# Kernel optimization log

Measured on AMD Instinct MI355X. Metric: run time of the kernel, lower is better.

Reference implementation:

```python
import jax, jax.numpy as jnp
import numpy as np

NUM_EXPERTS = 8
TOP_K = 2
HIDDEN = 2048
INTER = 5632
NUM_TOKENS = 8192


def setup_inputs() -> dict:
    key = jax.random.key(0)
    ks = jax.random.split(key, 5)
    s_h = 1.0 / np.sqrt(HIDDEN)
    s_i = 1.0 / np.sqrt(INTER)
    return {
        "hidden_states": jax.random.normal(ks[0], (NUM_TOKENS, HIDDEN), jnp.float32),
        # router: ReplicatedLinear(hidden, num_experts, bias=False) -> weight [E, H]
        "w_router": jax.random.normal(ks[1], (NUM_EXPERTS, HIDDEN), jnp.float32) * s_h,
        # FusedMoE SiLU-gated MLP per expert: gate/up [E, H, I], down [E, I, H]
        "w_gate": jax.random.normal(ks[2], (NUM_EXPERTS, HIDDEN, INTER), jnp.float32) * s_h,
        "w_up": jax.random.normal(ks[3], (NUM_EXPERTS, HIDDEN, INTER), jnp.float32) * s_h,
        "w_down": jax.random.normal(ks[4], (NUM_EXPERTS, INTER, HIDDEN), jnp.float32) * s_i,
    }


def reference(hidden_states, w_router, w_gate, w_up, w_down):
    x = hidden_states  # [T, H]
    # Router linear (no bias)
    router_logits = x @ w_router.T  # [T, E]
    # FusedMoE topk: softmax over all experts, take top-k, renormalize=False
    probs = jax.nn.softmax(router_logits.astype(jnp.float32), axis=-1)
    topk_w, topk_idx = jax.lax.top_k(probs, TOP_K)  # [T, k]
    topk_w = topk_w.astype(x.dtype)

    out = jnp.zeros_like(x)
    for e in range(NUM_EXPERTS):
        # combine weight for tokens that routed to expert e (0 otherwise)
        w_e = jnp.sum(jnp.where(topk_idx == e, topk_w, 0.0), axis=-1)  # [T]
        h = jax.nn.silu(x @ w_gate[e]) * (x @ w_up[e])  # [T, I]
        out = out + (h @ w_down[e]) * w_e[:, None]
    return out
```

## Files before the change

kernel.cpp:

```cpp
#include <hip/hip_runtime.h>
#include <hip/hip_bf16.h>
#include <cstdint>

#define NTOK 8192
#define NEXP 8
#define HID  2048
#define INTR 5632
#define NT1  44
#define NT2  16

#define TCNT_OFF    4096u
#define SLOT_OFF    65536u
#define T2S_OFF     262144u
#define W2_OFF      393216u
#define LISTS_OFF   524288u
#define WL_OFF      786432u
#define WG_OFF      2097152u
#define WBYTES      184549376u
#define WU_OFF      (WG_OFF + WBYTES)
#define HF_OFF      (WU_OFF + WBYTES)
#define HFBYTES     207618048u
#define XG_OFF      (HF_OFF + HFBYTES)

typedef float f32x4  __attribute__((ext_vector_type(4)));
typedef short s16x8  __attribute__((ext_vector_type(8)));
typedef short s16x4  __attribute__((ext_vector_type(4)));

__device__ __forceinline__ short bfc(float f) {
  __hip_bfloat16 h = __float2bfloat16(f);
  return __builtin_bit_cast(short, h);
}
__device__ __forceinline__ float b2f(short s) {
  unsigned u = ((unsigned)(unsigned short)s) << 16;
  return __builtin_bit_cast(float, u);
}
__device__ __forceinline__ s16x8 pk8(float4 a, float4 b) {
  s16x8 v;
  v[0]=bfc(a.x); v[1]=bfc(a.y); v[2]=bfc(a.z); v[3]=bfc(a.w);
  v[4]=bfc(b.x); v[5]=bfc(b.y); v[6]=bfc(b.z); v[7]=bfc(b.w);
  return v;
}
__device__ __forceinline__ void gload16(const void* g, void* l) {
  __builtin_amdgcn_global_load_lds((const __attribute__((address_space(1))) void*)g,
                                   (__attribute__((address_space(3))) void*)l, 16, 0, 0);
}

#define DSR128(dst, addr, IMM) \
  asm volatile("ds_read_b128 %0, %1 offset:" IMM : "=v"(dst) : "v"(addr))
#define WAITLGKM(N) do { \
  asm volatile("s_waitcnt lgkmcnt(" #N ")" ::: "memory"); \
  __builtin_amdgcn_sched_barrier(0); } while (0)
#define WAITVM(N) do { \
  asm volatile("s_waitcnt vmcnt(" #N ")" ::: "memory"); \
  __builtin_amdgcn_sched_barrier(0); } while (0)

#define LOADA4(D0, D1, D2, D3, PTR) \
  asm volatile("global_load_dwordx4 %0, %4, off\n\t" \
               "global_load_dwordx4 %1, %4, off offset:1024\n\t" \
               "global_load_dwordx4 %2, %4, off offset:2048\n\t" \
               "global_load_dwordx4 %3, %4, off offset:3072" \
               : "=&v"(D0), "=&v"(D1), "=&v"(D2), "=&v"(D3) : "v"(PTR))

#define MFMA_BF16 __builtin_amdgcn_mfma_f32_16x16x32_bf16

__global__ __launch_bounds__(256, 4) void prep_kernel(
    const float* __restrict__ src, short* __restrict__ dst,
    int KT, int NP, int Nsrc) {
  __shared__ float tile[32 * 132];
  const int b = blockIdx.x;
  const int np = b % NP;
  const int kt = (b / NP) % KT;
  const int e  = b / (NP * KT);
  const int tid = threadIdx.x;
  const float* s = src + (size_t)e * KT * 32 * (size_t)Nsrc + (size_t)kt * 32 * Nsrc + np * 128;
#pragma unroll
  for (int i = 0; i < 4; i++) {
    const int idx = tid + i * 256;
    const int row = idx >> 5, c4 = idx & 31;
    float4 v = *(const float4*)(s + (size_t)row * Nsrc + c4 * 4);
    *(float4*)(tile + row * 132 + c4 * 4) = v;
  }
  __syncthreads();
  short* dbase = dst + ((size_t)(e * KT + kt) * (NP * 8) + np * 8) * 512;
#pragma unroll
  for (int i = 0; i < 2; i++) {
    const int c = tid + i * 256;
    const int lane = c & 63;
    const int nf = c >> 6;
    const int n = nf * 16 + (lane & 15);
    const int kb = (lane >> 4) * 8;
    s16x8 o;
#pragma unroll
    for (int j = 0; j < 8; j++) o[j] = bfc(tile[(kb + j) * 132 + n]);
    *(s16x8*)(dbase + (size_t)c * 8) = o;
  }
}

__global__ void router_kernel(const float* __restrict__ x, const float* __restrict__ wr,
                              int* __restrict__ cnt, int* __restrict__ lists,
                              float* __restrict__ wlists) {
  const int wave = threadIdx.x >> 6;
  const int lane = threadIdx.x & 63;
  const int t = blockIdx.x * 4 + wave;
  if (t >= NTOK) return;
  float acc[NEXP];
#pragma unroll
  for (int e = 0; e < NEXP; e++) acc[e] = 0.f;
  const float* xrow = x + (size_t)t * HID;
#pragma unroll
  for (int j = 0; j < HID / 256; j++) {
    const int k = j * 256 + lane * 4;
    float4 xv = *(const float4*)(xrow + k);
#pragma unroll
    for (int e = 0; e < NEXP; e++) {
      float4 wv = *(const float4*)(wr + e * HID + k);
      acc[e] += xv.x * wv.x + xv.y * wv.y + xv.z * wv.z + xv.w * wv.w;
    }
  }
#pragma unroll
  for (int e = 0; e < NEXP; e++) {
    float v = acc[e];
    for (int off = 32; off; off >>= 1) v += __shfl_xor(v, off, 64);
    acc[e] = v;
  }
  if (lane == 0) {
    float m = acc[0];
#pragma unroll
    for (int e = 1; e < NEXP; e++) m = fmaxf(m, acc[e]);
    float p[NEXP], s = 0.f;
#pragma unroll
    for (int e = 0; e < NEXP; e++) { p[e] = __expf(acc[e] - m); s += p[e]; }
    const float inv = 1.f / s;
    int e1 = 0; float b1 = p[0];
#pragma unroll
    for (int e = 1; e < NEXP; e++) if (p[e] > b1) { b1 = p[e]; e1 = e; }
    int e2 = -1; float b2 = -1.f;
#pragma unroll
    for (int e = 0; e < NEXP; e++) if (e != e1 && p[e] > b2) { b2 = p[e]; e2 = e; }
    const int pos1 = atomicAdd(&cnt[e1], 1);
    lists[e1 * NTOK + pos1] = t; wlists[e1 * NTOK + pos1] = b1 * inv;
    const int pos2 = atomicAdd(&cnt[e2], 1);
    lists[e2 * NTOK + pos2] = t; wlists[e2 * NTOK + pos2] = b2 * inv;
  }
}

__global__ void offsets_kernel(const int* __restrict__ cnt, int* __restrict__ poffs) {
  if (threadIdx.x == 0 && blockIdx.x == 0) {
    int o = 0;
#pragma unroll
    for (int e = 0; e < NEXP; e++) { poffs[e] = o; o += ((cnt[e] + 255) >> 8) << 8; }
    poffs[NEXP] = o;
  }
}

__global__ void slotmap_kernel(const int* __restrict__ cnt, const int* __restrict__ poffs,
                               const int* __restrict__ lists, const float* __restrict__ wlists,
                               int* __restrict__ slotlist, int* __restrict__ tcnt,
                               int* __restrict__ tok2slot, float* __restrict__ w2) {
  const int e = blockIdx.x;
  const int c = cnt[e], base = poffs[e];
  for (int pos = threadIdx.x; pos < c; pos += blockDim.x) {
    const int tok = lists[e * NTOK + pos];
    const int slot = base + pos;
    slotlist[slot] = tok;
    const int j = atomicAdd(&tcnt[tok], 1);
    tok2slot[tok * 2 + j] = slot;
    w2[tok * 2 + j] = wlists[e * NTOK + pos];
  }
}

__global__ __launch_bounds__(256, 4) void gather_kernel(
    const float* __restrict__ x, const int* __restrict__ slotlist,
    short* __restrict__ xg) {
  const int c = blockIdx.x * 256 + threadIdx.x;
  const int cl = c & 63;
  const int fragid = c >> 6;
  const int f = fragid & 15;
  const int kt = (fragid >> 4) & 63;
  const int gmt = fragid >> 10;
  const int tok = slotlist[gmt * 256 + f * 16 + (cl & 15)];
  const float* s = x + (size_t)tok * HID + kt * 32 + (cl >> 4) * 8;
  float4 a = *(const float4*)s, b = *(const float4*)(s + 4);
  *(s16x8*)(xg + (size_t)c * 8) = pk8(a, b);
}

__global__ __launch_bounds__(512, 2) void gemm1_kernel(
    const short* __restrict__ xg, const short* __restrict__ wgb,
    const short* __restrict__ wub, const int* __restrict__ cnt,
    const int* __restrict__ poffs, short* __restrict__ hfrag) {
  const int P = blockIdx.x;
  const int xcd = P & 7, slot = P >> 3;
  const int mt = slot & 31, jj = slot >> 5;
  const int g = jj * 8 + xcd;
  const int e = g / NT1, nt = g % NT1;
  if (mt * 256 >= cnt[e]) return;
  const int gmt = (poffs[e] >> 8) + mt;
  const int tid = threadIdx.x;
  const int w = tid >> 6, lane = tid & 63;
  const int wm = w >> 1, wn = w & 1;

  __shared__ __align__(16) short Lds[34816];
  const uint32_t ldsbase = (uint32_t)(uintptr_t)&Lds[0];

  const short* srcA  = xg + (size_t)gmt * 64 * 16 * 512 + (size_t)(wm * 4) * 512 + lane * 8;
  const short* srcBg = wgb + (((size_t)e * 64) * 352 + nt * 8) * 512 + tid * 8;
  const short* srcBu = wub + (((size_t)e * 64) * 352 + nt * 8) * 512 + tid * 8;

  const uint32_t roB = wn * 4096 + lane * 16;
  const uint32_t roU = 8192 + wn * 4096 + lane * 16;

  f32x4 accG[4][4], accU[4][4];
#pragma unroll
  for (int i = 0; i < 4; i++)
#pragma unroll
    for (int j = 0; j < 4; j++) {
      accG[i][j] = f32x4{0.f, 0.f, 0.f, 0.f};
      accU[i][j] = f32x4{0.f, 0.f, 0.f, 0.f};
    }

  s16x8 arA0, arA1, arA2, arA3, arB0, arB1, arB2, arB3;

#define STG1(WB) do {                                                           \
    short* d = (short*)Lds + ((WB) >> 1);                                       \
    gload16(srcBg, d + w * 512);                                                \
    gload16(srcBu, d + 4096 + w * 512);                                         \
    srcBg += 180224; srcBu += 180224; } while (0)

#define MMQ1(NF, BG, BU, A0, A1, A2, A3)                                        \
  { __builtin_amdgcn_s_setprio(1);                                              \
    accG[0][NF] = MFMA_BF16(A0, BG, accG[0][NF], 0, 0, 0);                      \
    accU[0][NF] = MFMA_BF16(A0, BU, accU[0][NF], 0, 0, 0);                      \
    accG[1][NF] = MFMA_BF16(A1, BG, accG[1][NF], 0, 0, 0);                      \
    accU[1][NF] = MFMA_BF16(A1, BU, accU[1][NF], 0, 0, 0);                      \
    accG[2][NF] = MFMA_BF16(A2, BG, accG[2][NF], 0, 0, 0);                      \
    accU[2][NF] = MFMA_BF16(A2, BU, accU[2][NF], 0, 0, 0);                      \
    accG[3][NF] = MFMA_BF16(A3, BG, accG[3][NF], 0, 0, 0);                      \
    accU[3][NF] = MFMA_BF16(A3, BU, accU[3][NF], 0, 0, 0);                      \
    __builtin_amdgcn_s_setprio(0); }

#define G1_BODY(RB, WB, U0, U1, U2, U3, L0, L1, L2, L3, VTOP, VMID, DO_A, DO_STG) \
  {                                                                             \
    WAITVM(VTOP);                                                               \
    __builtin_amdgcn_s_barrier();                                               \
    const uint32_t rb = ldsbase + (RB);                                         \
    s16x8 bg0, bg1, bg2, bg3, bu0, bu1, bu2, bu3;                               \
    DSR128(bg0, rb + roB, "0");    DSR128(bu0, rb + roU, "0");                  \
    DSR128(bg1, rb + roB, "1024"); DSR128(bu1, rb + roU, "1024");               \
    DSR128(bg2, rb + roB, "2048"); DSR128(bu2, rb + roU, "2048");               \
    DSR128(bg3, rb + roB, "3072"); DSR128(bu3, rb + roU, "3072");               \
    if (DO_A) { LOADA4(L0, L1, L2, L3, srcA); srcA += 8192; }                   \
    if (DO_STG) { STG1(WB); }                                                   \
    WAITVM(VMID);                                                               \
    WAITLGKM(6);                                                                \
    MMQ1(0, bg0, bu0, U0, U1, U2, U3)                                           \
    WAITLGKM(4);                                                                \
    MMQ1(1, bg1, bu1, U0, U1, U2, U3)                                           \
    WAITLGKM(2);                                                                \
    MMQ1(2, bg2, bu2, U0, U1, U2, U3)                                           \
    WAITLGKM(0);                                                                \
    MMQ1(3, bg3, bu3, U0, U1, U2, U3)                                           \
  }

  STG1(0);
  LOADA4(arA0, arA1, arA2, arA3, srcA); srcA += 8192;
  STG1(16384);

  for (int it = 0; it < 10; ++it) {
    G1_BODY(0,     32768, arA0,arA1,arA2,arA3, arB0,arB1,arB2,arB3, 6, 8, 1, 1)
    G1_BODY(16384, 0,     arB0,arB1,arB2,arB3, arA0,arA1,arA2,arA3, 6, 8, 1, 1)
    G1_BODY(32768, 16384, arA0,arA1,arA2,arA3, arB0,arB1,arB2,arB3, 6, 8, 1, 1)
    G1_BODY(0,     32768, arB0,arB1,arB2,arB3, arA0,arA1,arA2,arA3, 6, 8, 1, 1)
    G1_BODY(16384, 0,     arA0,arA1,arA2,arA3, arB0,arB1,arB2,arB3, 6, 8, 1, 1)
    G1_BODY(32768, 16384, arB0,arB1,arB2,arB3, arA0,arA1,arA2,arA3, 6, 8, 1, 1)
  }
  G1_BODY(0,     32768, arA0,arA1,arA2,arA3, arB0,arB1,arB2,arB3, 6, 8, 1, 1)
  G1_BODY(16384, 0,     arB0,arB1,arB2,arB3, arA0,arA1,arA2,arA3, 6, 8, 1, 1)
  G1_BODY(32768, 0,     arA0,arA1,arA2,arA3, arB0,arB1,arB2,arB3, 6, 6, 1, 0)
  G1_BODY(0,     0,     arB0,arB1,arB2,arB3, arA0,arA1,arA2,arA3, 4, 0, 0, 0)
#undef G1_BODY
#undef MMQ1
#undef STG1

  short* tr = (short*)Lds;
  __syncthreads();
#pragma unroll
  for (int mf = 0; mf < 4; mf++)
#pragma unroll
    for (int reg = 0; reg < 4; reg++) {
      const int row = wm * 64 + mf * 16 + (lane >> 4) * 4 + reg;
#pragma unroll
      for (int nf = 0; nf < 4; nf++) {
        const int col = wn * 64 + nf * 16 + (lane & 15);
        const float gv = accG[mf][nf][reg];
        const float uv = accU[mf][nf][reg];
        tr[row * 136 + col] = bfc((gv / (1.f + __expf(-gv))) * uv);
      }
    }
  __syncthreads();
  short* hb = hfrag + (((size_t)gmt * 176 + nt * 4) * 16) * 512;
#pragma unroll
  for (int i = 0; i < 8; i++) {
    const int c = tid + i * 512;
    const int cl = c & 63;
    const int f = (c >> 6) & 15;
    const int ktl = c >> 10;
    const int rr = f * 16 + (cl & 15);
    s16x8 v = *(const s16x8*)(tr + rr * 136 + ktl * 32 + (cl >> 4) * 8);
    *(s16x8*)(hb + ((size_t)ktl * 16 + f) * 512 + cl * 8) = v;
  }
}

__global__ __launch_bounds__(512, 4) void gemm2_kernel(
    const short* __restrict__ hfrag, const short* __restrict__ wdb,
    const int* __restrict__ cnt, const int* __restrict__ poffs,
    __hip_bfloat16* __restrict__ pout) {
  const int P = blockIdx.x;
  const int xcd = P & 7, r = P >> 3;
  const int nt = r & 15, emq = r >> 4;
  const int gm = emq * 8 + xcd;
  const int e = gm >> 5, mt = gm & 31;
  if (mt * 256 >= cnt[e]) return;
  const int gmt = (poffs[e] >> 8) + mt;
  const int n0 = nt * 128;
  const int tid = threadIdx.x;
  const int w = tid >> 6, lane = tid & 63;
  const int wm = w >> 1, wn = w & 1;

  __shared__ __align__(16) short Lds[3 * 12288];
  const uint32_t ldsbase = (uint32_t)(uintptr_t)&Lds[0];

  const short* srcA = hfrag + (size_t)gmt * 176 * 16 * 512 + tid * 8;
  const short* srcB = wdb + (((size_t)e * 176) * 128 + nt * 8) * 512 + tid * 8;

  const uint32_t roA = wm * 4096 + lane * 16;
  const uint32_t roB = 16384 + wn * 4096 + lane * 16;

  f32x4 acc[4][4];
#pragma unroll
  for (int i = 0; i < 4; i++)
#pragma unroll
    for (int j = 0; j < 4; j++) acc[i][j] = f32x4{0.f, 0.f, 0.f, 0.f};

#define STG2(WB) do {                                                           \
    short* d = (short*)Lds + ((WB) >> 1);                                       \
    gload16(srcA,        d + w * 512);                                          \
    gload16(srcA + 4096, d + 4096 + w * 512);                                   \
    gload16(srcB,        d + 8192 + w * 512);                                   \
    srcA += 8192; srcB += 65536; } while (0)

#define MMQ2(NF, BF)                                                            \
  { __builtin_amdgcn_s_setprio(1);                                              \
    acc[0][NF] = MFMA_BF16(af0, BF, acc[0][NF], 0, 0, 0);                       \
    acc[1][NF] = MFMA_BF16(af1, BF, acc[1][NF], 0, 0, 0);                       \
    acc[2][NF] = MFMA_BF16(af2, BF, acc[2][NF], 0, 0, 0);                       \
    acc[3][NF] = MFMA_BF16(af3, BF, acc[3][NF], 0, 0, 0);                       \
    __builtin_amdgcn_s_setprio(0); }

#define G2_BODY(RB, WB, VMN, DOSTG)                                             \
  {                                                                             \
    WAITVM(VMN);                                                                \
    __builtin_amdgcn_s_barrier();                                               \
    const uint32_t rb = ldsbase + (RB);                                         \
    s16x8 af0, af1, af2, af3, bf0, bf1, bf2, bf3;                               \
    DSR128(bf0, rb + roB, "0");                                                 \
    DSR128(af0, rb + roA, "0");    DSR128(af1, rb + roA, "1024");               \
    DSR128(af2, rb + roA, "2048"); DSR128(af3, rb + roA, "3072");               \
    DSR128(bf1, rb + roB, "1024");                                              \
    DSR128(bf2, rb + roB, "2048");                                              \
    DSR128(bf3, rb + roB, "3072");                                              \
    if (DOSTG) { STG2(WB); }                                                    \
    WAITLGKM(3);                                                                \
    MMQ2(0, bf0)                                                                \
    WAITLGKM(2);                                                                \
    MMQ2(1, bf1)                                                                \
    WAITLGKM(1);                                                                \
    MMQ2(2, bf2)                                                                \
    WAITLGKM(0);                                                                \
    MMQ2(3, bf3)                                                                \
  }

  STG2(0);
  STG2(24576);
  for (int it = 0; it < 58; ++it) {
    G2_BODY(0,     49152, 3, 1)
    G2_BODY(24576, 0,     3, 1)
    G2_BODY(49152, 24576, 3, 1)
  }
  G2_BODY(0,     0, 3, 0)
  G2_BODY(24576, 0, 0, 0)
#undef G2_BODY
#undef MMQ2
#undef STG2

  const int slotb = poffs[e] + mt * 256;
#pragma unroll
  for (int mf = 0; mf < 4; mf++) {
#pragma unroll
    for (int reg = 0; reg < 4; reg++) {
      const int row = wm * 64 + mf * 16 + (lane >> 4) * 4 + reg;
      __hip_bfloat16* op = pout + (size_t)(slotb + row) * HID + n0 + wn * 64 + (lane & 15);
#pragma unroll
      for (int nf = 0; nf < 4; nf++)
        op[nf * 16] = __float2bfloat16(acc[mf][nf][reg]);
    }
  }
}

__global__ __launch_bounds__(256, 8) void combine_kernel(
    const __hip_bfloat16* __restrict__ pout, const int* __restrict__ tok2slot,
    const float* __restrict__ w2, float* __restrict__ out) {
  const int t = blockIdx.x;
  const int s0 = tok2slot[2 * t], s1 = tok2slot[2 * t + 1];
  const float w0 = w2[2 * t], w1 = w2[2 * t + 1];
  const short* p0 = (const short*)pout + (size_t)s0 * HID;
  const short* p1 = (const short*)pout + (size_t)s1 * HID;
  float* o = out + (size_t)t * HID;
  const int i = threadIdx.x;
  s16x8 a = *(const s16x8*)(p0 + i * 8);
  s16x8 b = *(const s16x8*)(p1 + i * 8);
  float4 r0, r1;
  r0.x = w0 * b2f(a[0]) + w1 * b2f(b[0]);
  r0.y = w0 * b2f(a[1]) + w1 * b2f(b[1]);
  r0.z = w0 * b2f(a[2]) + w1 * b2f(b[2]);
  r0.w = w0 * b2f(a[3]) + w1 * b2f(b[3]);
  r1.x = w0 * b2f(a[4]) + w1 * b2f(b[4]);
  r1.y = w0 * b2f(a[5]) + w1 * b2f(b[5]);
  r1.z = w0 * b2f(a[6]) + w1 * b2f(b[6]);
  r1.w = w0 * b2f(a[7]) + w1 * b2f(b[7]);
  *(float4*)(o + i * 8) = r0;
  *(float4*)(o + i * 8 + 4) = r1;
}

extern "C" void kernel_launch(void* const* d_in, const int* in_sizes, int n_in,
                              void* d_out, int out_size, void* d_ws, size_t ws_size,
                              hipStream_t stream) {
  const float* x  = (const float*)d_in[0];
  const float* wr = (const float*)d_in[1];
  const float* wg = (const float*)d_in[2];
  const float* wu = (const float*)d_in[3];
  const float* wd = (const float*)d_in[4];
  float* out = (float*)d_out;
  char* ws = (char*)d_ws;

  int* cnt      = (int*)ws;
  int* poffs    = (int*)(ws + 64);
  int* tcnt     = (int*)(ws + TCNT_OFF);
  int* slotlist = (int*)(ws + SLOT_OFF);
  int* tok2slot = (int*)(ws + T2S_OFF);
  float* w2     = (float*)(ws + W2_OFF);
  int* lists    = (int*)(ws + LISTS_OFF);
  float* wlists = (float*)(ws + WL_OFF);
  short* wgb    = (short*)(ws + WG_OFF);
  short* wub    = (short*)(ws + WU_OFF);
  short* wdb    = (short*)(ws + WG_OFF);
  short* hfrag  = (short*)(ws + HF_OFF);
  short* xg     = (short*)(ws + XG_OFF);
  __hip_bfloat16* pout = (__hip_bfloat16*)(ws + XG_OFF);

  hipMemsetAsync(ws, 0, 256, stream);
  hipMemsetAsync(ws + TCNT_OFF, 0, 32768, stream);
  hipMemsetAsync(ws + SLOT_OFF, 0, 73728, stream);

  router_kernel<<<NTOK / 4, 256, 0, stream>>>(x, wr, cnt, lists, wlists);
  offsets_kernel<<<1, 64, 0, stream>>>(cnt, poffs);
  slotmap_kernel<<<NEXP, 256, 0, stream>>>(cnt, poffs, lists, wlists, slotlist, tcnt, tok2slot, w2);
  gather_kernel<<<18432, 256, 0, stream>>>(x, slotlist, xg);
  prep_kernel<<<NEXP * 64 * 44, 256, 0, stream>>>(wg, wgb, 64, 44, INTR);
  prep_kernel<<<NEXP * 64 * 44, 256, 0, stream>>>(wu, wub, 64, 44, INTR);
  gemm1_kernel<<<8 * 32 * NT1, 512, 0, stream>>>(xg, wgb, wub, cnt, poffs, hfrag);
  prep_kernel<<<NEXP * 176 * 16, 256, 0, stream>>>(wd, wdb, 176, 16, HID);
  gemm2_kernel<<<8 * 16 * 32, 512, 0, stream>>>(hfrag, wdb, cnt, poffs, pout);
  combine_kernel<<<NTOK, 256, 0, stream>>>(pout, tok2slot, w2, out);
}
```

Measured before the change: 1.677 ms.

## Double wavefronts per block in both MoE GEMMs, halving per-wave N tile

Both grouped GEMM kernels now launch 1024 threads (16 waves) instead of 512. Each wave computes a 64x32 output slice instead of 64x64, which halves accumulator registers and B-fragment LDS reads per wave. gemm2 now loads A directly from global memory into registers, as gemm1 already does, instead of staging it in LDS, which shrinks its LDS buffers. The aim is more resident waves for latency hiding, at the cost of more redundant A loads, more barrier participants, and lower MFMA work per wave relative to LDS traffic.

```diff
diff --git a/kernel.cpp b/kernel.cpp
--- a/kernel.cpp
+++ b/kernel.cpp
@@ -184,7 +184,7 @@
   *(s16x8*)(xg + (size_t)c * 8) = pk8(a, b);
 }
 
-__global__ __launch_bounds__(512, 2) void gemm1_kernel(
+__global__ __launch_bounds__(1024, 4) void gemm1_kernel(
     const short* __restrict__ xg, const short* __restrict__ wgb,
     const short* __restrict__ wub, const int* __restrict__ cnt,
     const int* __restrict__ poffs, short* __restrict__ hfrag) {
@@ -197,23 +197,24 @@
   const int gmt = (poffs[e] >> 8) + mt;
   const int tid = threadIdx.x;
   const int w = tid >> 6, lane = tid & 63;
-  const int wm = w >> 1, wn = w & 1;
+  const int wm = w >> 2, wn = w & 3;
 
   __shared__ __align__(16) short Lds[34816];
   const uint32_t ldsbase = (uint32_t)(uintptr_t)&Lds[0];
 
-  const short* srcA  = xg + (size_t)gmt * 64 * 16 * 512 + (size_t)(wm * 4) * 512 + lane * 8;
-  const short* srcBg = wgb + (((size_t)e * 64) * 352 + nt * 8) * 512 + tid * 8;
-  const short* srcBu = wub + (((size_t)e * 64) * 352 + nt * 8) * 512 + tid * 8;
-
-  const uint32_t roB = wn * 4096 + lane * 16;
-  const uint32_t roU = 8192 + wn * 4096 + lane * 16;
-
-  f32x4 accG[4][4], accU[4][4];
+  const short* srcA = xg + (size_t)gmt * 64 * 16 * 512 + (size_t)(wm * 4) * 512 + lane * 8;
+  const int stid = tid & 511;
+  const short* srcB = ((tid < 512) ? wgb : wub)
+                    + (((size_t)e * 64) * 352 + nt * 8) * 512 + stid * 8;
+
+  const uint32_t roB = wn * 2048 + lane * 16;
+  const uint32_t roU = 8192 + wn * 2048 + lane * 16;
+
+  f32x4 accG[4][2], accU[4][2];
 #pragma unroll
   for (int i = 0; i < 4; i++)
 #pragma unroll
-    for (int j = 0; j < 4; j++) {
+    for (int j = 0; j < 2; j++) {
       accG[i][j] = f32x4{0.f, 0.f, 0.f, 0.f};
       accU[i][j] = f32x4{0.f, 0.f, 0.f, 0.f};
     }
@@ -221,10 +222,8 @@
   s16x8 arA0, arA1, arA2, arA3, arB0, arB1, arB2, arB3;
 
 #define STG1(WB) do {                                                           \
-    short* d = (short*)Lds + ((WB) >> 1);                                       \
-    gload16(srcBg, d + w * 512);                                                \
-    gload16(srcBu, d + 4096 + w * 512);                                         \
-    srcBg += 180224; srcBu += 180224; } while (0)
+    gload16(srcB, (short*)Lds + ((WB) >> 1) + tid * 8);                         \
+    srcB += 180224; } while (0)
 
 #define MMQ1(NF, BG, BU, A0, A1, A2, A3)                                        \
   { __builtin_amdgcn_s_setprio(1);                                              \
@@ -238,27 +237,20 @@
     accU[3][NF] = MFMA_BF16(A3, BU, accU[3][NF], 0, 0, 0);                      \
     __builtin_amdgcn_s_setprio(0); }
 
-#define G1_BODY(RB, WB, U0, U1, U2, U3, L0, L1, L2, L3, VTOP, VMID, DO_A, DO_STG) \
+#define G1_BODY(RB, WB, U0, U1, U2, U3, L0, L1, L2, L3, VTOP, DO_A, DO_STG)     \
   {                                                                             \
     WAITVM(VTOP);                                                               \
     __builtin_amdgcn_s_barrier();                                               \
     const uint32_t rb = ldsbase + (RB);                                         \
-    s16x8 bg0, bg1, bg2, bg3, bu0, bu1, bu2, bu3;                               \
+    s16x8 bg0, bg1, bu0, bu1;                                                   \
     DSR128(bg0, rb + roB, "0");    DSR128(bu0, rb + roU, "0");                  \
     DSR128(bg1, rb + roB, "1024"); DSR128(bu1, rb + roU, "1024");               \
-    DSR128(bg2, rb + roB, "2048"); DSR128(bu2, rb + roU, "2048");               \
-    DSR128(bg3, rb + roB, "3072"); DSR128(bu3, rb + roU, "3072");               \
     if (DO_A) { LOADA4(L0, L1, L2, L3, srcA); srcA += 8192; }                   \
     if (DO_STG) { STG1(WB); }                                                   \
-    WAITVM(VMID);                                                               \
-    WAITLGKM(6);                                                                \
+    WAITLGKM(2);                                                                \
     MMQ1(0, bg0, bu0, U0, U1, U2, U3)                                           \
-    WAITLGKM(4);                                                                \
+    WAITLGKM(0);                                                                \
     MMQ1(1, bg1, bu1, U0, U1, U2, U3)                                           \
-    WAITLGKM(2);                                                                \
-    MMQ1(2, bg2, bu2, U0, U1, U2, U3)                                           \
-    WAITLGKM(0);                                                                \
-    MMQ1(3, bg3, bu3, U0, U1, U2, U3)                                           \
   }
 
   STG1(0);
@@ -266,17 +258,17 @@
   STG1(16384);
 
   for (int it = 0; it < 10; ++it) {
-    G1_BODY(0,     32768, arA0,arA1,arA2,arA3, arB0,arB1,arB2,arB3, 6, 8, 1, 1)
-    G1_BODY(16384, 0,     arB0,arB1,arB2,arB3, arA0,arA1,arA2,arA3, 6, 8, 1, 1)
-    G1_BODY(32768, 16384, arA0,arA1,arA2,arA3, arB0,arB1,arB2,arB3, 6, 8, 1, 1)
-    G1_BODY(0,     32768, arB0,arB1,arB2,arB3, arA0,arA1,arA2,arA3, 6, 8, 1, 1)
-    G1_BODY(16384, 0,     arA0,arA1,arA2,arA3, arB0,arB1,arB2,arB3, 6, 8, 1, 1)
-    G1_BODY(32768, 16384, arB0,arB1,arB2,arB3, arA0,arA1,arA2,arA3, 6, 8, 1, 1)
-  }
-  G1_BODY(0,     32768, arA0,arA1,arA2,arA3, arB0,arB1,arB2,arB3, 6, 8, 1, 1)
-  G1_BODY(16384, 0,     arB0,arB1,arB2,arB3, arA0,arA1,arA2,arA3, 6, 8, 1, 1)
-  G1_BODY(32768, 0,     arA0,arA1,arA2,arA3, arB0,arB1,arB2,arB3, 6, 6, 1, 0)
-  G1_BODY(0,     0,     arB0,arB1,arB2,arB3, arA0,arA1,arA2,arA3, 4, 0, 0, 0)
+    G1_BODY(0,     32768, arA0,arA1,arA2,arA3, arB0,arB1,arB2,arB3, 1, 1, 1)
+    G1_BODY(16384, 0,     arB0,arB1,arB2,arB3, arA0,arA1,arA2,arA3, 1, 1, 1)
+    G1_BODY(32768, 16384, arA0,arA1,arA2,arA3, arB0,arB1,arB2,arB3, 1, 1, 1)
+    G1_BODY(0,     32768, arB0,arB1,arB2,arB3, arA0,arA1,arA2,arA3, 1, 1, 1)
+    G1_BODY(16384, 0,     arA0,arA1,arA2,arA3, arB0,arB1,arB2,arB3, 1, 1, 1)
+    G1_BODY(32768, 16384, arB0,arB1,arB2,arB3, arA0,arA1,arA2,arA3, 1, 1, 1)
+  }
+  G1_BODY(0,     32768, arA0,arA1,arA2,arA3, arB0,arB1,arB2,arB3, 1, 1, 1)
+  G1_BODY(16384, 0,     arB0,arB1,arB2,arB3, arA0,arA1,arA2,arA3, 1, 1, 1)
+  G1_BODY(32768, 0,     arA0,arA1,arA2,arA3, arB0,arB1,arB2,arB3, 1, 1, 0)
+  G1_BODY(0,     0,     arB0,arB1,arB2,arB3, arA0,arA1,arA2,arA3, 0, 0, 0)
 #undef G1_BODY
 #undef MMQ1
 #undef STG1
@@ -289,8 +281,8 @@
     for (int reg = 0; reg < 4; reg++) {
       const int row = wm * 64 + mf * 16 + (lane >> 4) * 4 + reg;
 #pragma unroll
-      for (int nf = 0; nf < 4; nf++) {
-        const int col = wn * 64 + nf * 16 + (lane & 15);
+      for (int nf = 0; nf < 2; nf++) {
+        const int col = wn * 32 + nf * 16 + (lane & 15);
         const float gv = accG[mf][nf][reg];
         const float uv = accU[mf][nf][reg];
         tr[row * 136 + col] = bfc((gv / (1.f + __expf(-gv))) * uv);
@@ -299,8 +291,8 @@
   __syncthreads();
   short* hb = hfrag + (((size_t)gmt * 176 + nt * 4) * 16) * 512;
 #pragma unroll
-  for (int i = 0; i < 8; i++) {
-    const int c = tid + i * 512;
+  for (int i = 0; i < 4; i++) {
+    const int c = tid + i * 1024;
     const int cl = c & 63;
     const int f = (c >> 6) & 15;
     const int ktl = c >> 10;
@@ -310,7 +302,7 @@
   }
 }
 
-__global__ __launch_bounds__(512, 4) void gemm2_kernel(
+__global__ __launch_bounds__(1024, 4) void gemm2_kernel(
     const short* __restrict__ hfrag, const short* __restrict__ wdb,
     const int* __restrict__ cnt, const int* __restrict__ poffs,
     __hip_bfloat16* __restrict__ pout) {
@@ -324,70 +316,68 @@
   const int n0 = nt * 128;
   const int tid = threadIdx.x;
   const int w = tid >> 6, lane = tid & 63;
-  const int wm = w >> 1, wn = w & 1;
-
-  __shared__ __align__(16) short Lds[3 * 12288];
+  const int wm = w >> 2, wn = w & 3;
+  const bool w8 = (w < 8);
+
+  __shared__ __align__(16) short Lds[3 * 4096];
   const uint32_t ldsbase = (uint32_t)(uintptr_t)&Lds[0];
 
-  const short* srcA = hfrag + (size_t)gmt * 176 * 16 * 512 + tid * 8;
-  const short* srcB = wdb + (((size_t)e * 176) * 128 + nt * 8) * 512 + tid * 8;
-
-  const uint32_t roA = wm * 4096 + lane * 16;
-  const uint32_t roB = 16384 + wn * 4096 + lane * 16;
-
-  f32x4 acc[4][4];
+  const short* srcA = hfrag + (size_t)gmt * 176 * 16 * 512 + (size_t)(wm * 4) * 512 + lane * 8;
+  const int stid = tid & 511;
+  const short* srcB = wdb + (((size_t)e * 176) * 128 + nt * 8) * 512 + stid * 8;
+
+  const uint32_t roB = wn * 2048 + lane * 16;
+
+  f32x4 acc[4][2];
 #pragma unroll
   for (int i = 0; i < 4; i++)
 #pragma unroll
-    for (int j = 0; j < 4; j++) acc[i][j] = f32x4{0.f, 0.f, 0.f, 0.f};
+    for (int j = 0; j < 2; j++) acc[i][j] = f32x4{0.f, 0.f, 0.f, 0.f};
+
+  s16x8 arA0, arA1, arA2, arA3, arB0, arB1, arB2, arB3;
 
 #define STG2(WB) do {                                                           \
-    short* d = (short*)Lds + ((WB) >> 1);                                       \
-    gload16(srcA,        d + w * 512);                                          \
-    gload16(srcA + 4096, d + 4096 + w * 512);                                   \
-    gload16(srcB,        d + 8192 + w * 512);                                   \
-    srcA += 8192; srcB += 65536; } while (0)
-
-#define MMQ2(NF, BF)                                                            \
+    if (tid < 512) gload16(srcB, (short*)Lds + ((WB) >> 1) + tid * 8);          \
+    srcB += 65536; } while (0)
+
+#define MMQ2(NF, BF, A0, A1, A2, A3)                                            \
   { __builtin_amdgcn_s_setprio(1);                                              \
-    acc[0][NF] = MFMA_BF16(af0, BF, acc[0][NF], 0, 0, 0);                       \
-    acc[1][NF] = MFMA_BF16(af1, BF, acc[1][NF], 0, 0, 0);                       \
-    acc[2][NF] = MFMA_BF16(af2, BF, acc[2][NF], 0, 0, 0);                       \
-    acc[3][NF] = MFMA_BF16(af3, BF, acc[3][NF], 0, 0, 0);                       \
+    acc[0][NF] = MFMA_BF16(A0, BF, acc[0][NF], 0, 0, 0);                        \
+    acc[1][NF] = MFMA_BF16(A1, BF, acc[1][NF], 0, 0, 0);                        \
+    acc[2][NF] = MFMA_BF16(A2, BF, acc[2][NF], 0, 0, 0);                        \
+    acc[3][NF] = MFMA_BF16(A3, BF, acc[3][NF], 0, 0, 0);                        \
     __builtin_amdgcn_s_setprio(0); }
 
-#define G2_BODY(RB, WB, VMN, DOSTG)                                             \
+#define G2_BODY(RB, WB, U0, U1, U2, U3, L0, L1, L2, L3, VT, DO_A, DO_STG)       \
   {                                                                             \
-    WAITVM(VMN);                                                                \
+    if ((VT) && w8) { WAITVM(1); } else { WAITVM(0); }                          \
     __builtin_amdgcn_s_barrier();                                               \
     const uint32_t rb = ldsbase + (RB);                                         \
-    s16x8 af0, af1, af2, af3, bf0, bf1, bf2, bf3;                               \
+    s16x8 bf0, bf1;                                                             \
     DSR128(bf0, rb + roB, "0");                                                 \
-    DSR128(af0, rb + roA, "0");    DSR128(af1, rb + roA, "1024");               \
-    DSR128(af2, rb + roA, "2048"); DSR128(af3, rb + roA, "3072");               \
     DSR128(bf1, rb + roB, "1024");                                              \
-    DSR128(bf2, rb + roB, "2048");                                              \
-    DSR128(bf3, rb + roB, "3072");                                              \
-    if (DOSTG) { STG2(WB); }                                                    \
-    WAITLGKM(3);                                                                \
-    MMQ2(0, bf0)                                                                \
-    WAITLGKM(2);                                                                \
-    MMQ2(1, bf1)                                                                \
+    if (DO_A) { LOADA4(L0, L1, L2, L3, srcA); srcA += 8192; }                   \
+    if (DO_STG) { STG2(WB); }                                                   \
     WAITLGKM(1);                                                                \
-    MMQ2(2, bf2)                                                                \
+    MMQ2(0, bf0, U0, U1, U2, U3)                                                \
     WAITLGKM(0);                                                                \
-    MMQ2(3, bf3)                                                                \
+    MMQ2(1, bf1, U0, U1, U2, U3)                                                \
   }
 
   STG2(0);
-  STG2(24576);
-  for (int it = 0; it < 58; ++it) {
-    G2_BODY(0,     49152, 3, 1)
-    G2_BODY(24576, 0,     3, 1)
-    G2_BODY(49152, 24576, 3, 1)
-  }
-  G2_BODY(0,     0, 3, 0)
-  G2_BODY(24576, 0, 0, 0)
+  LOADA4(arA0, arA1, arA2, arA3, srcA); srcA += 8192;
+  STG2(8192);
+
+  for (int it = 0; it < 29; ++it) {
+    G2_BODY(0,     16384, arA0,arA1,arA2,arA3, arB0,arB1,arB2,arB3, 1, 1, 1)
+    G2_BODY(8192,  0,     arB0,arB1,arB2,arB3, arA0,arA1,arA2,arA3, 1, 1, 1)
+    G2_BODY(16384, 8192,  arA0,arA1,arA2,arA3, arB0,arB1,arB2,arB3, 1, 1, 1)
+    G2_BODY(0,     16384, arB0,arB1,arB2,arB3, arA0,arA1,arA2,arA3, 1, 1, 1)
+    G2_BODY(8192,  0,     arA0,arA1,arA2,arA3, arB0,arB1,arB2,arB3, 1, 1, 1)
+    G2_BODY(16384, 8192,  arB0,arB1,arB2,arB3, arA0,arA1,arA2,arA3, 1, 1, 1)
+  }
+  G2_BODY(0,     0, arA0,arA1,arA2,arA3, arB0,arB1,arB2,arB3, 1, 1, 0)
+  G2_BODY(8192,  0, arB0,arB1,arB2,arB3, arA0,arA1,arA2,arA3, 0, 0, 0)
 #undef G2_BODY
 #undef MMQ2
 #undef STG2
@@ -398,10 +388,9 @@
 #pragma unroll
     for (int reg = 0; reg < 4; reg++) {
       const int row = wm * 64 + mf * 16 + (lane >> 4) * 4 + reg;
-      __hip_bfloat16* op = pout + (size_t)(slotb + row) * HID + n0 + wn * 64 + (lane & 15);
-#pragma unroll
-      for (int nf = 0; nf < 4; nf++)
-        op[nf * 16] = __float2bfloat16(acc[mf][nf][reg]);
+      __hip_bfloat16* op = pout + (size_t)(slotb + row) * HID + n0 + wn * 32 + (lane & 15);
+      op[0]  = __float2bfloat16(acc[mf][0][reg]);
+      op[16] = __float2bfloat16(acc[mf][1][reg]);
     }
   }
 }
@@ -467,8 +456,8 @@
   gather_kernel<<<18432, 256, 0, stream>>>(x, slotlist, xg);
   prep_kernel<<<NEXP * 64 * 44, 256, 0, stream>>>(wg, wgb, 64, 44, INTR);
   prep_kernel<<<NEXP * 64 * 44, 256, 0, stream>>>(wu, wub, 64, 44, INTR);
-  gemm1_kernel<<<8 * 32 * NT1, 512, 0, stream>>>(xg, wgb, wub, cnt, poffs, hfrag);
+  gemm1_kernel<<<8 * 32 * NT1, 1024, 0, stream>>>(xg, wgb, wub, cnt, poffs, hfrag);
   prep_kernel<<<NEXP * 176 * 16, 256, 0, stream>>>(wd, wdb, 176, 16, HID);
-  gemm2_kernel<<<8 * 16 * 32, 512, 0, stream>>>(hfrag, wdb, cnt, poffs, pout);
+  gemm2_kernel<<<8 * 16 * 32, 1024, 0, stream>>>(hfrag, wdb, cnt, poffs, pout);
   combine_kernel<<<NTOK, 256, 0, stream>>>(pout, tok2slot, w2, out);
 }
```

New measurement: 2.811 ms. 67.5% more time.

## Stage A tiles through LDS and double K-step per barrier in gemm1

Applied to the files above, without the earlier changes.

Gemm1 no longer loads the A (token) fragments straight from global memory into registers. A is now staged through LDS with direct global-to-LDS loads next to the gate/up weight tiles, and each barrier stage covers two K sub-steps instead of one. The pipeline goes from a triple-buffered 16KB scheme to a double-buffered 64KB one, which halves the barrier count and interleaves LDS reads with MFMAs. The cost is a full 128KB of LDS per block, which can cut occupancy, plus a vmcnt(0) wait at each stage that may expose global-load latency.

```diff
diff --git a/kernel.cpp b/kernel.cpp
--- a/kernel.cpp
+++ b/kernel.cpp
@@ -53,13 +53,6 @@
 #define WAITVM(N) do { \
   asm volatile("s_waitcnt vmcnt(" #N ")" ::: "memory"); \
   __builtin_amdgcn_sched_barrier(0); } while (0)
-
-#define LOADA4(D0, D1, D2, D3, PTR) \
-  asm volatile("global_load_dwordx4 %0, %4, off\n\t" \
-               "global_load_dwordx4 %1, %4, off offset:1024\n\t" \
-               "global_load_dwordx4 %2, %4, off offset:2048\n\t" \
-               "global_load_dwordx4 %3, %4, off offset:3072" \
-               : "=&v"(D0), "=&v"(D1), "=&v"(D2), "=&v"(D3) : "v"(PTR))
 
 #define MFMA_BF16 __builtin_amdgcn_mfma_f32_16x16x32_bf16
 
@@ -199,15 +192,16 @@
   const int w = tid >> 6, lane = tid & 63;
   const int wm = w >> 1, wn = w & 1;
 
-  __shared__ __align__(16) short Lds[34816];
+  __shared__ __align__(16) short Lds[65536];
   const uint32_t ldsbase = (uint32_t)(uintptr_t)&Lds[0];
 
-  const short* srcA  = xg + (size_t)gmt * 64 * 16 * 512 + (size_t)(wm * 4) * 512 + lane * 8;
+  const short* srcA  = xg + (size_t)gmt * 64 * 16 * 512 + tid * 8;
   const short* srcBg = wgb + (((size_t)e * 64) * 352 + nt * 8) * 512 + tid * 8;
   const short* srcBu = wub + (((size_t)e * 64) * 352 + nt * 8) * 512 + tid * 8;
 
-  const uint32_t roB = wn * 4096 + lane * 16;
-  const uint32_t roU = 8192 + wn * 4096 + lane * 16;
+  const uint32_t roA = wm * 4096 + lane * 16;
+  const uint32_t roB = 32768 + wn * 4096 + lane * 16;
+  const uint32_t roU = 49152 + wn * 4096 + lane * 16;
 
   f32x4 accG[4][4], accU[4][4];
 #pragma unroll
@@ -218,65 +212,74 @@
       accU[i][j] = f32x4{0.f, 0.f, 0.f, 0.f};
     }
 
-  s16x8 arA0, arA1, arA2, arA3, arB0, arB1, arB2, arB3;
-
 #define STG1(WB) do {                                                           \
     short* d = (short*)Lds + ((WB) >> 1);                                       \
-    gload16(srcBg, d + w * 512);                                                \
-    gload16(srcBu, d + 4096 + w * 512);                                         \
-    srcBg += 180224; srcBu += 180224; } while (0)
-
-#define MMQ1(NF, BG, BU, A0, A1, A2, A3)                                        \
+    gload16(srcA,          d + tid * 8);                                        \
+    gload16(srcA + 4096,   d + 4096 + tid * 8);                                 \
+    gload16(srcA + 8192,   d + 8192 + tid * 8);                                 \
+    gload16(srcA + 12288,  d + 12288 + tid * 8);                                \
+    gload16(srcBg,            d + 16384 + tid * 8);                             \
+    gload16(srcBg + 180224,   d + 20480 + tid * 8);                             \
+    gload16(srcBu,            d + 24576 + tid * 8);                             \
+    gload16(srcBu + 180224,   d + 28672 + tid * 8);                             \
+    srcA += 16384; srcBg += 360448; srcBu += 360448; } while (0)
+
+#define MMQ1(NF, BG, BU, A)                                                     \
   { __builtin_amdgcn_s_setprio(1);                                              \
-    accG[0][NF] = MFMA_BF16(A0, BG, accG[0][NF], 0, 0, 0);                      \
-    accU[0][NF] = MFMA_BF16(A0, BU, accU[0][NF], 0, 0, 0);                      \
-    accG[1][NF] = MFMA_BF16(A1, BG, accG[1][NF], 0, 0, 0);                      \
-    accU[1][NF] = MFMA_BF16(A1, BU, accU[1][NF], 0, 0, 0);                      \
-    accG[2][NF] = MFMA_BF16(A2, BG, accG[2][NF], 0, 0, 0);                      \
-    accU[2][NF] = MFMA_BF16(A2, BU, accU[2][NF], 0, 0, 0);                      \
-    accG[3][NF] = MFMA_BF16(A3, BG, accG[3][NF], 0, 0, 0);                      \
-    accU[3][NF] = MFMA_BF16(A3, BU, accU[3][NF], 0, 0, 0);                      \
+    accG[0][NF] = MFMA_BF16(A[0], BG[NF], accG[0][NF], 0, 0, 0);                \
+    accU[0][NF] = MFMA_BF16(A[0], BU[NF], accU[0][NF], 0, 0, 0);                \
+    accG[1][NF] = MFMA_BF16(A[1], BG[NF], accG[1][NF], 0, 0, 0);                \
+    accU[1][NF] = MFMA_BF16(A[1], BU[NF], accU[1][NF], 0, 0, 0);                \
+    accG[2][NF] = MFMA_BF16(A[2], BG[NF], accG[2][NF], 0, 0, 0);                \
+    accU[2][NF] = MFMA_BF16(A[2], BU[NF], accU[2][NF], 0, 0, 0);                \
+    accG[3][NF] = MFMA_BF16(A[3], BG[NF], accG[3][NF], 0, 0, 0);                \
+    accU[3][NF] = MFMA_BF16(A[3], BU[NF], accU[3][NF], 0, 0, 0);                \
     __builtin_amdgcn_s_setprio(0); }
 
-#define G1_BODY(RB, WB, U0, U1, U2, U3, L0, L1, L2, L3, VTOP, VMID, DO_A, DO_STG) \
+#define G1_BODY(RB, WB, DO_STG)                                                 \
   {                                                                             \
-    WAITVM(VTOP);                                                               \
+    WAITVM(0);                                                                  \
     __builtin_amdgcn_s_barrier();                                               \
     const uint32_t rb = ldsbase + (RB);                                         \
-    s16x8 bg0, bg1, bg2, bg3, bu0, bu1, bu2, bu3;                               \
-    DSR128(bg0, rb + roB, "0");    DSR128(bu0, rb + roU, "0");                  \
-    DSR128(bg1, rb + roB, "1024"); DSR128(bu1, rb + roU, "1024");               \
-    DSR128(bg2, rb + roB, "2048"); DSR128(bu2, rb + roU, "2048");               \
-    DSR128(bg3, rb + roB, "3072"); DSR128(bu3, rb + roU, "3072");               \
-    if (DO_A) { LOADA4(L0, L1, L2, L3, srcA); srcA += 8192; }                   \
+    s16x8 a0[4], bg0[4], bu0[4], a1[4], bg1[4], bu1[4];                         \
+    DSR128(bg0[0], rb + roB, "0");     DSR128(bu0[0], rb + roU, "0");           \
+    DSR128(a0[0], rb + roA, "0");      DSR128(a0[1], rb + roA, "1024");         \
+    DSR128(a0[2], rb + roA, "2048");   DSR128(a0[3], rb + roA, "3072");         \
+    DSR128(bg0[1], rb + roB, "1024");  DSR128(bu0[1], rb + roU, "1024");        \
+    DSR128(bg0[2], rb + roB, "2048");  DSR128(bu0[2], rb + roU, "2048");        \
+    DSR128(bg0[3], rb + roB, "3072");  DSR128(bu0[3], rb + roU, "3072");        \
     if (DO_STG) { STG1(WB); }                                                   \
-    WAITVM(VMID);                                                               \
     WAITLGKM(6);                                                                \
-    MMQ1(0, bg0, bu0, U0, U1, U2, U3)                                           \
+    MMQ1(0, bg0, bu0, a0)                                                       \
+    DSR128(bg1[0], rb + roB, "8192");  DSR128(bu1[0], rb + roU, "8192");        \
+    DSR128(a1[0], rb + roA, "16384");  DSR128(a1[1], rb + roA, "17408");        \
+    DSR128(a1[2], rb + roA, "18432");  DSR128(a1[3], rb + roA, "19456");        \
+    WAITLGKM(10);                                                               \
+    MMQ1(1, bg0, bu0, a0)                                                       \
+    DSR128(bg1[1], rb + roB, "9216");  DSR128(bu1[1], rb + roU, "9216");        \
+    DSR128(bg1[2], rb + roB, "10240"); DSR128(bu1[2], rb + roU, "10240");       \
+    DSR128(bg1[3], rb + roB, "11264"); DSR128(bu1[3], rb + roU, "11264");       \
+    WAITLGKM(14);                                                               \
+    MMQ1(2, bg0, bu0, a0)                                                       \
+    WAITLGKM(12);                                                               \
+    MMQ1(3, bg0, bu0, a0)                                                       \
+    WAITLGKM(6);                                                                \
+    MMQ1(0, bg1, bu1, a1)                                                       \
     WAITLGKM(4);                                                                \
-    MMQ1(1, bg1, bu1, U0, U1, U2, U3)                                           \
+    MMQ1(1, bg1, bu1, a1)                                                       \
     WAITLGKM(2);                                                                \
-    MMQ1(2, bg2, bu2, U0, U1, U2, U3)                                           \
+    MMQ1(2, bg1, bu1, a1)                                                       \
     WAITLGKM(0);                                                                \
-    MMQ1(3, bg3, bu3, U0, U1, U2, U3)                                           \
+    MMQ1(3, bg1, bu1, a1)                                                       \
   }
 
   STG1(0);
-  LOADA4(arA0, arA1, arA2, arA3, srcA); srcA += 8192;
-  STG1(16384);
-
-  for (int it = 0; it < 10; ++it) {
-    G1_BODY(0,     32768, arA0,arA1,arA2,arA3, arB0,arB1,arB2,arB3, 6, 8, 1, 1)
-    G1_BODY(16384, 0,     arB0,arB1,arB2,arB3, arA0,arA1,arA2,arA3, 6, 8, 1, 1)
-    G1_BODY(32768, 16384, arA0,arA1,arA2,arA3, arB0,arB1,arB2,arB3, 6, 8, 1, 1)
-    G1_BODY(0,     32768, arB0,arB1,arB2,arB3, arA0,arA1,arA2,arA3, 6, 8, 1, 1)
-    G1_BODY(16384, 0,     arA0,arA1,arA2,arA3, arB0,arB1,arB2,arB3, 6, 8, 1, 1)
-    G1_BODY(32768, 16384, arB0,arB1,arB2,arB3, arA0,arA1,arA2,arA3, 6, 8, 1, 1)
-  }
-  G1_BODY(0,     32768, arA0,arA1,arA2,arA3, arB0,arB1,arB2,arB3, 6, 8, 1, 1)
-  G1_BODY(16384, 0,     arB0,arB1,arB2,arB3, arA0,arA1,arA2,arA3, 6, 8, 1, 1)
-  G1_BODY(32768, 0,     arA0,arA1,arA2,arA3, arB0,arB1,arB2,arB3, 6, 6, 1, 0)
-  G1_BODY(0,     0,     arB0,arB1,arB2,arB3, arA0,arA1,arA2,arA3, 4, 0, 0, 0)
+  for (int it = 0; it < 15; ++it) {
+    G1_BODY(0,     65536, 1)
+    G1_BODY(65536, 0,     1)
+  }
+  G1_BODY(0,     65536, 1)
+  G1_BODY(65536, 0,     0)
 #undef G1_BODY
 #undef MMQ1
 #undef STG1
@@ -457,9 +460,9 @@
   short* xg     = (short*)(ws + XG_OFF);
   __hip_bfloat16* pout = (__hip_bfloat16*)(ws + XG_OFF);
 
-  hipMemsetAsync(ws, 0, 256, stream);
-  hipMemsetAsync(ws + TCNT_OFF, 0, 32768, stream);
-  hipMemsetAsync(ws + SLOT_OFF, 0, 73728, stream);
+  (void)hipMemsetAsync(ws, 0, 256, stream);
+  (void)hipMemsetAsync(ws + TCNT_OFF, 0, 32768, stream);
+  (void)hipMemsetAsync(ws + SLOT_OFF, 0, 73728, stream);
 
   router_kernel<<<NTOK / 4, 256, 0, stream>>>(x, wr, cnt, lists, wlists);
   offsets_kernel<<<1, 64, 0, stream>>>(cnt, poffs);
```

New measurement: 1.709 ms. Within noise of the previous version (+1.9%).
